# Kernel optimization log

Hardware: AMD Instinct MI355X
Metric: run time of the kernel (lower is better)

Reference implementation:

```python
import jax, jax.numpy as jnp
import numpy as np

B, T, D, H = 2, 2048, 2048, 16
HS = D // H  # head size 128


def setup_inputs() -> dict:
    key = jax.random.key(0)
    ks = jax.random.split(key, 5)
    s = 0.02
    return {
        "x": jax.random.normal(ks[0], (B, T, D), dtype=jnp.float32),
        "wq": jax.random.normal(ks[1], (D, D), dtype=jnp.float32) * s,
        "wk": jax.random.normal(ks[2], (D, D), dtype=jnp.float32) * s,
        "wv": jax.random.normal(ks[3], (D, D), dtype=jnp.float32) * s,
        "wo": jax.random.normal(ks[4], (D, D), dtype=jnp.float32) * s,
    }


def reference(x, wq, wk, wv, wo):
    b, t, d = x.shape
    # projections: nn.Linear(x) = x @ W.T ; here W stored as (out,in)
    q = (x @ wq.T).reshape(b, t, H, HS).transpose(0, 2, 1, 3)  # (B,H,T,HS)
    k = (x @ wk.T).reshape(b, t, H, HS).transpose(0, 2, 1, 3)
    v = (x @ wv.T).reshape(b, t, H, HS).transpose(0, 2, 1, 3)
    scale = 1.0 / np.sqrt(HS).astype(np.float32)
    e = jnp.einsum("bhqd,bhkd->bhqk", q, k) * scale  # (B,H,T,T)
    causal = jnp.tril(jnp.ones((t, t), dtype=bool))
    e = jnp.where(causal[None, None], e, jnp.float32(-jnp.inf))
    alpha = jax.nn.softmax(e, axis=-1)  # dropout=0.0 -> identity
    attn = jnp.einsum("bhqk,bhkd->bhqd", alpha, v)
    attn = attn.transpose(0, 2, 1, 3).reshape(b, t, d)
    return attn @ wo.T
```

## Files before the change

### kernel.cpp

```cpp
#include <hip/hip_runtime.h>
#include <hip/hip_bf16.h>

typedef __bf16 bf16x8 __attribute__((ext_vector_type(8)));
typedef float f32x4 __attribute__((ext_vector_type(4)));
typedef unsigned short u16x8 __attribute__((ext_vector_type(8)));

#define GLDS16(g, s)                                                         \
  __builtin_amdgcn_global_load_lds(                                          \
      (const __attribute__((address_space(1))) void*)(g),                    \
      (__attribute__((address_space(3))) void*)(s), 16, 0, 0)

__device__ __forceinline__ void store1(__hip_bfloat16* p, float v) { *p = __float2bfloat16(v); }
__device__ __forceinline__ void store1(float* p, float v) { *p = v; }

__global__ __launch_bounds__(256) void cast_f32_to_bf16(const float4* __restrict__ in,
                                                        ushort4* __restrict__ out, int n4) {
  int i = blockIdx.x * 256 + threadIdx.x;
  if (i >= n4) return;
  float4 v = in[i];
  union { ushort4 u; __hip_bfloat16 h[4]; } o;
  o.h[0] = __float2bfloat16(v.x);
  o.h[1] = __float2bfloat16(v.y);
  o.h[2] = __float2bfloat16(v.z);
  o.h[3] = __float2bfloat16(v.w);
  out[i] = o.u;
}

__global__ __launch_bounds__(256) void cast4_f32_to_bf16(const float4* __restrict__ w0,
                                                         const float4* __restrict__ w1,
                                                         const float4* __restrict__ w2,
                                                         const float4* __restrict__ w3,
                                                         ushort4* __restrict__ o0,
                                                         ushort4* __restrict__ o1,
                                                         ushort4* __restrict__ o2,
                                                         ushort4* __restrict__ o3, int n4) {
  int i = blockIdx.x * 256 + threadIdx.x;
  if (i >= n4) return;
  int s = blockIdx.y;
  const float4* in = (s == 0) ? w0 : (s == 1) ? w1 : (s == 2) ? w2 : w3;
  ushort4* out = (s == 0) ? o0 : (s == 1) ? o1 : (s == 2) ? o2 : o3;
  float4 v = in[i];
  union { ushort4 u; __hip_bfloat16 h[4]; } o;
  o.h[0] = __float2bfloat16(v.x);
  o.h[1] = __float2bfloat16(v.y);
  o.h[2] = __float2bfloat16(v.z);
  o.h[3] = __float2bfloat16(v.w);
  out[i] = o.u;
}

template <typename OutT>
__global__ __launch_bounds__(512, 2) void gemm256(const __hip_bfloat16* __restrict__ A,
                                                  const __hip_bfloat16* __restrict__ B0,
                                                  const __hip_bfloat16* __restrict__ B1,
                                                  const __hip_bfloat16* __restrict__ B2,
                                                  OutT* __restrict__ C0,
                                                  OutT* __restrict__ C1,
                                                  OutT* __restrict__ C2,
                                                  int nBx, int nBy, int ntPerMat,
                                                  int N, int K) {
  __shared__ __hip_bfloat16 As[3][128 * 64];
  __shared__ __hip_bfloat16 Bs[3][256 * 64];

  const int t = threadIdx.x;
  const int w = t >> 6, l = t & 63;
  const int lr = l & 15, hi = l >> 4;

  const int nwg = nBx * nBy;
  int id = (int)blockIdx.x;
  id = (id & 7) * (nwg >> 3) + (id >> 3);
  const int bx = id / nBy;
  const int by = id % nBy;

  const int sel = bx / ntPerMat;
  const __hip_bfloat16* Bm = (sel == 0) ? B0 : ((sel == 1) ? B1 : B2);
  OutT* Cm = (sel == 0) ? C0 : ((sel == 1) ? C1 : C2);
  const int n0 = (bx - sel * ntPerMat) * 256;
  const int m0 = by * 128;

  const int c0r = t >> 3, cs = t & 7;
  const int c1r = 64 + c0r;
  const __hip_bfloat16* aP0 = A + (size_t)(m0 + c0r) * K + (cs ^ (c0r & 7)) * 8;
  const __hip_bfloat16* aP1 = A + (size_t)(m0 + c1r) * K + (cs ^ (c1r & 7)) * 8;
  const __hip_bfloat16* bP0 = Bm + (size_t)(n0 + c0r) * K + (cs ^ (c0r & 7)) * 8;
  const __hip_bfloat16* bP1 = Bm + (size_t)(n0 + c1r) * K + (cs ^ (c1r & 7)) * 8;
  const size_t HK = (size_t)128 * K;

#define STAGE_T(bb, koff)                                                    \
  do {                                                                       \
    GLDS16(aP0 + (koff), (char*)As[bb] + t * 16);                            \
    GLDS16(aP1 + (koff), (char*)As[bb] + 8192 + t * 16);                     \
    GLDS16(bP0 + (koff), (char*)Bs[bb] + t * 16);                            \
    GLDS16(bP1 + (koff), (char*)Bs[bb] + 8192 + t * 16);                     \
    GLDS16(bP0 + HK + (koff), (char*)Bs[bb] + 16384 + t * 16);               \
    GLDS16(bP1 + HK + (koff), (char*)Bs[bb] + 24576 + t * 16);               \
  } while (0)

  f32x4 acc[2][4][2] = {};
  bf16x8 afA[4][2];
  bf16x8 bqA[2][2], bqB[2][2];
  const int NT = K / 64;
  const int sw = lr & 7;
  const int arow = (w >> 2) * 64;
  const int brow = (w & 3) * 32;

#define RD_A(dst)                                                            \
  _Pragma("unroll") for (int mi = 0; mi < 4; ++mi)                           \
    _Pragma("unroll") for (int kk = 0; kk < 2; ++kk)                         \
      dst[mi][kk] = *(const bf16x8*)((const char*)As[buf] +                  \
          (arow + mi * 16 + lr) * 128 + (((kk * 4 + hi) ^ sw) << 4));
#define RD_B(dst, nh)                                                        \
  _Pragma("unroll") for (int ni = 0; ni < 2; ++ni)                           \
    _Pragma("unroll") for (int kk = 0; kk < 2; ++kk)                         \
      dst[ni][kk] = *(const bf16x8*)((const char*)Bs[buf] +                  \
          ((nh) * 128 + brow + ni * 16 + lr) * 128 + (((kk * 4 + hi) ^ sw) << 4));
#define MFMA_Q(nh, afv, bq)                                                  \
  do {                                                                       \
    __builtin_amdgcn_s_setprio(1);                                           \
    _Pragma("unroll") for (int mi = 0; mi < 4; ++mi)                         \
      _Pragma("unroll") for (int ni = 0; ni < 2; ++ni) {                     \
        acc[nh][mi][ni] = __builtin_amdgcn_mfma_f32_16x16x32_bf16(           \
            afv[mi][0], bq[ni][0], acc[nh][mi][ni], 0, 0, 0);                \
        acc[nh][mi][ni] = __builtin_amdgcn_mfma_f32_16x16x32_bf16(           \
            afv[mi][1], bq[ni][1], acc[nh][mi][ni], 0, 0, 0);                \
      }                                                                      \
    __builtin_amdgcn_s_setprio(0);                                           \
  } while (0)
#define WAITV(n)  asm volatile("s_waitcnt vmcnt(" #n ")" ::: "memory")

  STAGE_T(0, 0);
  STAGE_T(1, 64);

  for (int tt = 0; tt < NT; ++tt) {
    const int buf = tt % 3;

    if (tt + 1 < NT) WAITV(6); else WAITV(0);
    __builtin_amdgcn_s_barrier();

    RD_A(afA);
    RD_B(bqA, 0);
    RD_B(bqB, 1);
    if (tt + 2 < NT) STAGE_T((tt + 2) % 3, (size_t)(tt + 2) * 64);

    MFMA_Q(0, afA, bqA);
    MFMA_Q(1, afA, bqB);
  }
#undef WAITV
#undef MFMA_Q
#undef RD_B
#undef RD_A
#undef STAGE_T

#pragma unroll
  for (int nh = 0; nh < 2; ++nh)
#pragma unroll
    for (int mi = 0; mi < 4; ++mi)
#pragma unroll
      for (int ni = 0; ni < 2; ++ni)
#pragma unroll
        for (int i = 0; i < 4; ++i) {
          size_t idx = (size_t)(m0 + arow + mi * 16 + hi * 4 + i) * N +
                       (n0 + nh * 128 + brow + ni * 16 + lr);
          store1(&Cm[idx], acc[nh][mi][ni][i]);
        }
}

__global__ __launch_bounds__(256, 2) void flash_attn(const __hip_bfloat16* __restrict__ Qg,
                                                     const __hip_bfloat16* __restrict__ Kg,
                                                     const __hip_bfloat16* __restrict__ Vg,
                                                     __hip_bfloat16* __restrict__ Og) {
  __shared__ __hip_bfloat16 Ks[2][64 * 128];
  __shared__ __hip_bfloat16 Vt[128 * 64];

  const int mblk = blockIdx.x;
  const int bh = mblk & 31;
  const int jj = mblk >> 5;
  const int qt = (jj < 8) ? (15 - jj) : (jj - 8);
  const int b = bh >> 4, h = bh & 15;
  const int q0 = qt * 128;
  const int t = threadIdx.x, w = t >> 6, l = t & 63;
  const int lr = l & 15, hi = l >> 4;
  const size_t base = ((size_t)b * 2048) * 2048 + (size_t)h * 128;
  const int nt = 2 * qt + 2;
  const float scale = 0.08838834764831843f;

  const int hi2 = (hi & 1) * 2;
  const int addrA = (((hi2) << 4) | lr) << 2;
  const int addrB = (((hi2 + 1) << 4) | lr) << 2;
  int addr_o[4];
#pragma unroll
  for (int i = 0; i < 4; ++i) addr_o[i] = ((l & 48) | (hi * 4 + i)) << 2;
  const bool hiHigh = (hi >> 1) != 0;

  bf16x8 qf[2][4];
#pragma unroll
  for (int g = 0; g < 2; ++g) {
    const __hip_bfloat16* qrow = Qg + base + (size_t)(q0 + w * 32 + g * 16 + lr) * 2048;
#pragma unroll
    for (int kk = 0; kk < 4; ++kk)
      qf[g][kk] = *(const bf16x8*)(qrow + kk * 32 + hi * 8);
  }

  f32x4 o_acc[2][8] = {};
  float m_run[2] = {-1e30f, -1e30f};
  float l_run[2] = {0.f, 0.f};

  const __hip_bfloat16* kptr[4];
#pragma unroll
  for (int i = 0; i < 4; ++i) {
    int c = i * 256 + t;
    int kr = c >> 4;
    int ke = ((c & 15) ^ (kr & 7)) * 8;
    kptr[i] = Kg + base + (size_t)kr * 2048 + ke;
  }
  const __hip_bfloat16* vptr[2];
#pragma unroll
  for (int it = 0; it < 2; ++it) {
    int kp = it * 16 + w * 4 + hi;
    vptr[it] = Vg + base + (size_t)(kp * 2) * 2048 + lr * 8;
  }

  u16x8 va[2], vb[2];
#pragma unroll
  for (int i = 0; i < 4; ++i)
    GLDS16(kptr[i], (char*)Ks[0] + (i * 256 + t) * 16);
#pragma unroll
  for (int it = 0; it < 2; ++it) {
    va[it] = *(const u16x8*)vptr[it];
    vb[it] = *(const u16x8*)(vptr[it] + 2048);
  }

  for (int kt = 0; kt < nt; ++kt) {
    const int cur = kt & 1;
    const int kb = kt * 64;
    __syncthreads();

#pragma unroll
    for (int it = 0; it < 2; ++it)
#pragma unroll
      for (int j2 = 0; j2 < 8; ++j2) {
        int d = lr * 8 + j2;
        int sw = (lr ^ j2) & 7;
        int off = d * 128 + (((it * 4 + w) ^ sw) << 4) + hi * 4;
        *(unsigned int*)((char*)Vt + off) =
            (unsigned int)va[it][j2] | ((unsigned int)vb[it][j2] << 16);
      }
    if (kt + 1 < nt) {
      const size_t adv = (size_t)(kb + 64) * 2048;
#pragma unroll
      for (int i = 0; i < 4; ++i)
        GLDS16(kptr[i] + adv, (char*)Ks[cur ^ 1] + (i * 256 + t) * 16);
#pragma unroll
      for (int it = 0; it < 2; ++it) {
        va[it] = *(const u16x8*)(vptr[it] + adv);
        vb[it] = *(const u16x8*)(vptr[it] + adv + 2048);
      }
    }
    asm volatile("s_waitcnt lgkmcnt(0)" ::: "memory");
    __builtin_amdgcn_s_barrier();

    if (!(kt == nt - 1 && w < 2)) {
      const char* ks = (const char*)Ks[cur];

      f32x4 st[2][4];
#pragma unroll
      for (int g = 0; g < 2; ++g)
#pragma unroll
        for (int nk = 0; nk < 4; ++nk) { f32x4 z = {}; st[g][nk] = z; }
#pragma unroll
      for (int nk = 0; nk < 4; ++nk)
#pragma unroll
        for (int kk = 0; kk < 4; ++kk) {
          bf16x8 kf = *(const bf16x8*)(ks + (nk * 16 + lr) * 256 +
                                       (((kk * 4 + hi) ^ (lr & 7)) << 4));
#pragma unroll
          for (int g = 0; g < 2; ++g)
            st[g][nk] = __builtin_amdgcn_mfma_f32_16x16x32_bf16(kf, qf[g][kk], st[g][nk], 0, 0, 0);
        }

      const bool maskt = (kt >= nt - 2);
#pragma unroll
      for (int g = 0; g < 2; ++g)
#pragma unroll
        for (int nk = 0; nk < 4; ++nk)
#pragma unroll
          for (int i = 0; i < 4; ++i) {
            float v = st[g][nk][i] * scale;
            if (maskt) {
              int ki = kb + nk * 16 + hi * 4 + i;
              int qi = q0 + w * 32 + g * 16 + lr;
              if (ki > qi) v = -1e30f;
            }
            st[g][nk][i] = v;
          }

      bf16x8 paf[2][2];
#pragma unroll
      for (int g = 0; g < 2; ++g) {
        float t0 = fmaxf(fmaxf(st[g][0][0], st[g][0][1]), fmaxf(st[g][0][2], st[g][0][3]));
        float t1 = fmaxf(fmaxf(st[g][1][0], st[g][1][1]), fmaxf(st[g][1][2], st[g][1][3]));
        float t2 = fmaxf(fmaxf(st[g][2][0], st[g][2][1]), fmaxf(st[g][2][2], st[g][2][3]));
        float t3 = fmaxf(fmaxf(st[g][3][0], st[g][3][1]), fmaxf(st[g][3][2], st[g][3][3]));
        float mx = fmaxf(fmaxf(t0, t1), fmaxf(t2, t3));
        mx = fmaxf(mx, __shfl_xor(mx, 16));
        mx = fmaxf(mx, __shfl_xor(mx, 32));

        if (!__all(mx - m_run[g] <= 8.0f)) {
          float mnew = fmaxf(m_run[g], mx);
          float rs = __expf(m_run[g] - mnew);
          m_run[g] = mnew;
          l_run[g] *= rs;
          int rsi = __float_as_int(rs);
#pragma unroll
          for (int i = 0; i < 4; ++i) {
            float rso = __int_as_float(__builtin_amdgcn_ds_bpermute(addr_o[i], rsi));
#pragma unroll
            for (int nc = 0; nc < 8; ++nc) o_acc[g][nc][i] *= rso;
          }
        }

#pragma unroll
        for (int nk = 0; nk < 4; ++nk)
#pragma unroll
          for (int i = 0; i < 4; ++i)
            st[g][nk][i] = __expf(st[g][nk][i] - m_run[g]);

        float s0 = (st[g][0][0] + st[g][0][1]) + (st[g][0][2] + st[g][0][3]);
        float s1 = (st[g][1][0] + st[g][1][1]) + (st[g][1][2] + st[g][1][3]);
        float s2 = (st[g][2][0] + st[g][2][1]) + (st[g][2][2] + st[g][2][3]);
        float s3 = (st[g][3][0] + st[g][3][1]) + (st[g][3][2] + st[g][3][3]);
        float sm = (s0 + s1) + (s2 + s3);
        sm += __shfl_xor(sm, 16);
        sm += __shfl_xor(sm, 32);
        l_run[g] += sm;

        unsigned pk[4][2];
#pragma unroll
        for (int nk = 0; nk < 4; ++nk) {
          asm("v_cvt_pk_bf16_f32 %0, %1, %2"
              : "=v"(pk[nk][0]) : "v"(st[g][nk][0]), "v"(st[g][nk][1]));
          asm("v_cvt_pk_bf16_f32 %0, %1, %2"
              : "=v"(pk[nk][1]) : "v"(st[g][nk][2]), "v"(st[g][nk][3]));
        }

#pragma unroll
        for (int kk = 0; kk < 2; ++kk) {
          unsigned au[4];
#pragma unroll
          for (int p = 0; p < 4; ++p) {
            int ad = (p < 2) ? addrA : addrB;
            int v0 = __builtin_amdgcn_ds_bpermute(ad, (int)pk[2 * kk][p & 1]);
            int v1 = __builtin_amdgcn_ds_bpermute(ad, (int)pk[2 * kk + 1][p & 1]);
            au[p] = hiHigh ? (unsigned)v1 : (unsigned)v0;
          }
          union { unsigned u[4]; bf16x8 v; } cv;
          cv.u[0] = au[0]; cv.u[1] = au[1]; cv.u[2] = au[2]; cv.u[3] = au[3];
          paf[g][kk] = cv.v;
        }
      }

#pragma unroll
      for (int kk = 0; kk < 2; ++kk)
#pragma unroll
        for (int nc = 0; nc < 8; ++nc) {
          int d = nc * 16 + lr;
          int sw = ((d >> 3) ^ d) & 7;
          bf16x8 vfr = *(const bf16x8*)((const char*)Vt + d * 128 +
                                        (((kk * 4 + hi) ^ sw) << 4));
#pragma unroll
          for (int g = 0; g < 2; ++g)
            o_acc[g][nc] = __builtin_amdgcn_mfma_f32_16x16x32_bf16(paf[g][kk], vfr, o_acc[g][nc], 0, 0, 0);
        }
    }
  }

#pragma unroll
  for (int g = 0; g < 2; ++g) {
    float lo[4];
#pragma unroll
    for (int i = 0; i < 4; ++i)
      lo[i] = __int_as_float(__builtin_amdgcn_ds_bpermute(addr_o[i], __float_as_int(l_run[g])));
#pragma unroll
    for (int nc = 0; nc < 8; ++nc)
#pragma unroll
      for (int i = 0; i < 4; ++i) {
        float val = o_acc[g][nc][i] / lo[i];
        Og[base + (size_t)(q0 + w * 32 + g * 16 + hi * 4 + i) * 2048 + nc * 16 + lr] =
            __float2bfloat16(val);
      }
  }
}

extern "C" void kernel_launch(void* const* d_in, const int* in_sizes, int n_in,
                              void* d_out, int out_size, void* d_ws, size_t ws_size,
                              hipStream_t stream) {
  const float* x  = (const float*)d_in[0];
  const float* wq = (const float*)d_in[1];
  const float* wk = (const float*)d_in[2];
  const float* wv = (const float*)d_in[3];
  const float* wo = (const float*)d_in[4];
  float* out = (float*)d_out;

  const int BT = 4096, D = 2048;
  const size_t ND = (size_t)D * D;
  const size_t NX = (size_t)BT * D;

  __hip_bfloat16* xb  = (__hip_bfloat16*)d_ws;
  __hip_bfloat16* wqb = xb + NX;
  __hip_bfloat16* wkb = wqb + ND;
  __hip_bfloat16* wvb = wkb + ND;
  __hip_bfloat16* wob = wvb + ND;
  __hip_bfloat16* Qb  = wob + ND;
  __hip_bfloat16* Kb  = Qb + NX;
  __hip_bfloat16* Vb  = Kb + NX;
  __hip_bfloat16* Ab  = Vb + NX;

  cast_f32_to_bf16<<<(int)(NX / 4 / 256), 256, 0, stream>>>((const float4*)x, (ushort4*)xb, (int)(NX / 4));
  cast4_f32_to_bf16<<<dim3((int)(ND / 4 / 256), 4), 256, 0, stream>>>(
      (const float4*)wq, (const float4*)wk, (const float4*)wv, (const float4*)wo,
      (ushort4*)wqb, (ushort4*)wkb, (ushort4*)wvb, (ushort4*)wob, (int)(ND / 4));

  gemm256<__hip_bfloat16><<<768, 512, 0, stream>>>(
      xb, wqb, wkb, wvb, Qb, Kb, Vb, 24, 32, 8, D, D);

  flash_attn<<<512, 256, 0, stream>>>(Qb, Kb, Vb, Ab);

  gemm256<float><<<256, 512, 0, stream>>>(
      Ab, wob, wob, wob, out, out, out, 8, 32, 8, D, D);
}
```

Measured before the change: 277.6 us.

## Software-pipeline QK^T in flash attention, simplify GEMM to double buffering, split QKV launches

The flash attention loop now computes the next tile's QK^T scores ahead of the softmax/PV work on the current tile. It double-buffers the V transpose in shared memory so the next V tile can be written while the current one is consumed. The GEMM drops from a 3-stage to a 2-stage LDS pipeline with a full vmcnt(0) wait each iteration, and the fused QKV launch is split into three separate launches. This trades more registers and LDS in attention, plus less load/compute overlap and extra launches in the GEMMs, for more overlap inside attention.

```diff
diff --git a/kernel.cpp b/kernel.cpp
--- a/kernel.cpp
+++ b/kernel.cpp
@@ -51,15 +51,10 @@
 template <typename OutT>
 __global__ __launch_bounds__(512, 2) void gemm256(const __hip_bfloat16* __restrict__ A,
                                                   const __hip_bfloat16* __restrict__ B0,
-                                                  const __hip_bfloat16* __restrict__ B1,
-                                                  const __hip_bfloat16* __restrict__ B2,
                                                   OutT* __restrict__ C0,
-                                                  OutT* __restrict__ C1,
-                                                  OutT* __restrict__ C2,
-                                                  int nBx, int nBy, int ntPerMat,
-                                                  int N, int K) {
-  __shared__ __hip_bfloat16 As[3][128 * 64];
-  __shared__ __hip_bfloat16 Bs[3][256 * 64];
+                                                  int nBx, int nBy, int N, int K) {
+  __shared__ __hip_bfloat16 As[2][128 * 64];
+  __shared__ __hip_bfloat16 Bs[2][256 * 64];
 
   const int t = threadIdx.x;
   const int w = t >> 6, l = t & 63;
@@ -71,18 +66,15 @@
   const int bx = id / nBy;
   const int by = id % nBy;
 
-  const int sel = bx / ntPerMat;
-  const __hip_bfloat16* Bm = (sel == 0) ? B0 : ((sel == 1) ? B1 : B2);
-  OutT* Cm = (sel == 0) ? C0 : ((sel == 1) ? C1 : C2);
-  const int n0 = (bx - sel * ntPerMat) * 256;
+  const int n0 = bx * 256;
   const int m0 = by * 128;
 
   const int c0r = t >> 3, cs = t & 7;
   const int c1r = 64 + c0r;
   const __hip_bfloat16* aP0 = A + (size_t)(m0 + c0r) * K + (cs ^ (c0r & 7)) * 8;
   const __hip_bfloat16* aP1 = A + (size_t)(m0 + c1r) * K + (cs ^ (c1r & 7)) * 8;
-  const __hip_bfloat16* bP0 = Bm + (size_t)(n0 + c0r) * K + (cs ^ (c0r & 7)) * 8;
-  const __hip_bfloat16* bP1 = Bm + (size_t)(n0 + c1r) * K + (cs ^ (c1r & 7)) * 8;
+  const __hip_bfloat16* bP0 = B0 + (size_t)(n0 + c0r) * K + (cs ^ (c0r & 7)) * 8;
+  const __hip_bfloat16* bP1 = B0 + (size_t)(n0 + c1r) * K + (cs ^ (c1r & 7)) * 8;
   const size_t HK = (size_t)128 * K;
 
 #define STAGE_T(bb, koff)                                                    \
@@ -128,19 +120,18 @@
 #define WAITV(n)  asm volatile("s_waitcnt vmcnt(" #n ")" ::: "memory")
 
   STAGE_T(0, 0);
-  STAGE_T(1, 64);
 
   for (int tt = 0; tt < NT; ++tt) {
-    const int buf = tt % 3;
-
-    if (tt + 1 < NT) WAITV(6); else WAITV(0);
+    const int buf = tt & 1, nb = buf ^ 1;
+    const bool stg = (tt + 1 < NT);
+    const size_t ko = (size_t)(tt + 1) * 64;
+
+    WAITV(0);
     __builtin_amdgcn_s_barrier();
-
     RD_A(afA);
     RD_B(bqA, 0);
     RD_B(bqB, 1);
-    if (tt + 2 < NT) STAGE_T((tt + 2) % 3, (size_t)(tt + 2) * 64);
-
+    if (stg) STAGE_T(nb, ko);
     MFMA_Q(0, afA, bqA);
     MFMA_Q(1, afA, bqB);
   }
@@ -160,7 +151,7 @@
         for (int i = 0; i < 4; ++i) {
           size_t idx = (size_t)(m0 + arow + mi * 16 + hi * 4 + i) * N +
                        (n0 + nh * 128 + brow + ni * 16 + lr);
-          store1(&Cm[idx], acc[nh][mi][ni][i]);
+          store1(&C0[idx], acc[nh][mi][ni][i]);
         }
 }
 
@@ -169,7 +160,7 @@
                                                      const __hip_bfloat16* __restrict__ Vg,
                                                      __hip_bfloat16* __restrict__ Og) {
   __shared__ __hip_bfloat16 Ks[2][64 * 128];
-  __shared__ __hip_bfloat16 Vt[128 * 64];
+  __shared__ __hip_bfloat16 Vt[2][128 * 64];
 
   const int mblk = blockIdx.x;
   const int bh = mblk & 31;
@@ -219,7 +210,32 @@
     vptr[it] = Vg + base + (size_t)(kp * 2) * 2048 + lr * 8;
   }
 
+#define WRITE_VT(vbuf, a, bmat)                                              \
+  _Pragma("unroll") for (int it = 0; it < 2; ++it)                           \
+    _Pragma("unroll") for (int j2 = 0; j2 < 8; ++j2) {                       \
+      int d = lr * 8 + j2;                                                   \
+      int swz = (lr ^ j2) & 7;                                               \
+      int off = d * 128 + (((it * 4 + w) ^ swz) << 4) + hi * 4;              \
+      *(unsigned int*)((char*)Vt[vbuf] + off) =                              \
+          (unsigned)a[it][j2] | ((unsigned)bmat[it][j2] << 16);              \
+    }
+#define QK_MFMA(dst, ksbuf)                                                  \
+  do {                                                                       \
+    const char* ks_ = (const char*)Ks[ksbuf];                                \
+    _Pragma("unroll") for (int g = 0; g < 2; ++g)                            \
+      _Pragma("unroll") for (int nk = 0; nk < 4; ++nk) { f32x4 z = {}; dst[g][nk] = z; } \
+    _Pragma("unroll") for (int nk = 0; nk < 4; ++nk)                         \
+      _Pragma("unroll") for (int kk = 0; kk < 4; ++kk) {                     \
+        bf16x8 kf = *(const bf16x8*)(ks_ + (nk * 16 + lr) * 256 +            \
+                                     (((kk * 4 + hi) ^ (lr & 7)) << 4));     \
+        _Pragma("unroll") for (int g = 0; g < 2; ++g)                        \
+          dst[g][nk] = __builtin_amdgcn_mfma_f32_16x16x32_bf16(kf, qf[g][kk], dst[g][nk], 0, 0, 0); \
+      }                                                                      \
+  } while (0)
+
   u16x8 va[2], vb[2];
+  f32x4 st[2][4];
+
 #pragma unroll
   for (int i = 0; i < 4; ++i)
     GLDS16(kptr[i], (char*)Ks[0] + (i * 256 + t) * 16);
@@ -228,55 +244,47 @@
     va[it] = *(const u16x8*)vptr[it];
     vb[it] = *(const u16x8*)(vptr[it] + 2048);
   }
+  asm volatile("s_waitcnt vmcnt(0)" ::: "memory");
+  __builtin_amdgcn_s_barrier();
+  WRITE_VT(0, va, vb);
+  if (nt > 1) {
+    const size_t adv = (size_t)64 * 2048;
+#pragma unroll
+    for (int i = 0; i < 4; ++i)
+      GLDS16(kptr[i] + adv, (char*)Ks[1] + (i * 256 + t) * 16);
+#pragma unroll
+    for (int it = 0; it < 2; ++it) {
+      va[it] = *(const u16x8*)(vptr[it] + adv);
+      vb[it] = *(const u16x8*)(vptr[it] + adv + 2048);
+    }
+  }
+  QK_MFMA(st, 0);
+  asm volatile("s_waitcnt lgkmcnt(0)" ::: "memory");
 
   for (int kt = 0; kt < nt; ++kt) {
-    const int cur = kt & 1;
     const int kb = kt * 64;
-    __syncthreads();
-
-#pragma unroll
-    for (int it = 0; it < 2; ++it)
-#pragma unroll
-      for (int j2 = 0; j2 < 8; ++j2) {
-        int d = lr * 8 + j2;
-        int sw = (lr ^ j2) & 7;
-        int off = d * 128 + (((it * 4 + w) ^ sw) << 4) + hi * 4;
-        *(unsigned int*)((char*)Vt + off) =
-            (unsigned int)va[it][j2] | ((unsigned int)vb[it][j2] << 16);
-      }
-    if (kt + 1 < nt) {
-      const size_t adv = (size_t)(kb + 64) * 2048;
+
+    asm volatile("s_waitcnt vmcnt(4)" ::: "memory");
+    __builtin_amdgcn_s_barrier();
+
+    if (kt + 1 < nt) { WRITE_VT((kt + 1) & 1, va, vb); }
+    if (kt + 2 < nt) {
+      const size_t adv = (size_t)(kb + 128) * 2048;
 #pragma unroll
       for (int i = 0; i < 4; ++i)
-        GLDS16(kptr[i] + adv, (char*)Ks[cur ^ 1] + (i * 256 + t) * 16);
+        GLDS16(kptr[i] + adv, (char*)Ks[kt & 1] + (i * 256 + t) * 16);
 #pragma unroll
       for (int it = 0; it < 2; ++it) {
         va[it] = *(const u16x8*)(vptr[it] + adv);
         vb[it] = *(const u16x8*)(vptr[it] + adv + 2048);
       }
     }
-    asm volatile("s_waitcnt lgkmcnt(0)" ::: "memory");
-    __builtin_amdgcn_s_barrier();
-
-    if (!(kt == nt - 1 && w < 2)) {
-      const char* ks = (const char*)Ks[cur];
-
-      f32x4 st[2][4];
-#pragma unroll
-      for (int g = 0; g < 2; ++g)
-#pragma unroll
-        for (int nk = 0; nk < 4; ++nk) { f32x4 z = {}; st[g][nk] = z; }
-#pragma unroll
-      for (int nk = 0; nk < 4; ++nk)
-#pragma unroll
-        for (int kk = 0; kk < 4; ++kk) {
-          bf16x8 kf = *(const bf16x8*)(ks + (nk * 16 + lr) * 256 +
-                                       (((kk * 4 + hi) ^ (lr & 7)) << 4));
-#pragma unroll
-          for (int g = 0; g < 2; ++g)
-            st[g][nk] = __builtin_amdgcn_mfma_f32_16x16x32_bf16(kf, qf[g][kk], st[g][nk], 0, 0, 0);
-        }
-
+
+    f32x4 stn[2][4];
+    if (kt + 1 < nt) { QK_MFMA(stn, (kt + 1) & 1); }
+
+    const bool active = !(kt == nt - 1 && w < 2);
+    if (active) {
       const bool maskt = (kt >= nt - 2);
 #pragma unroll
       for (int g = 0; g < 2; ++g)
@@ -363,13 +371,21 @@
 #pragma unroll
         for (int nc = 0; nc < 8; ++nc) {
           int d = nc * 16 + lr;
-          int sw = ((d >> 3) ^ d) & 7;
-          bf16x8 vfr = *(const bf16x8*)((const char*)Vt + d * 128 +
-                                        (((kk * 4 + hi) ^ sw) << 4));
+          int swz = ((d >> 3) ^ d) & 7;
+          bf16x8 vfr = *(const bf16x8*)((const char*)Vt[kt & 1] + d * 128 +
+                                        (((kk * 4 + hi) ^ swz) << 4));
 #pragma unroll
           for (int g = 0; g < 2; ++g)
             o_acc[g][nc] = __builtin_amdgcn_mfma_f32_16x16x32_bf16(paf[g][kk], vfr, o_acc[g][nc], 0, 0, 0);
         }
+    }
+
+    asm volatile("s_waitcnt lgkmcnt(0)" ::: "memory");
+    if (kt + 1 < nt) {
+#pragma unroll
+      for (int g = 0; g < 2; ++g)
+#pragma unroll
+        for (int nk = 0; nk < 4; ++nk) st[g][nk] = stn[g][nk];
     }
   }
 
@@ -388,6 +404,8 @@
             __float2bfloat16(val);
       }
   }
+#undef QK_MFMA
+#undef WRITE_VT
 }
 
 extern "C" void kernel_launch(void* const* d_in, const int* in_sizes, int n_in,
@@ -419,11 +437,11 @@
       (const float4*)wq, (const float4*)wk, (const float4*)wv, (const float4*)wo,
       (ushort4*)wqb, (ushort4*)wkb, (ushort4*)wvb, (ushort4*)wob, (int)(ND / 4));
 
-  gemm256<__hip_bfloat16><<<768, 512, 0, stream>>>(
-      xb, wqb, wkb, wvb, Qb, Kb, Vb, 24, 32, 8, D, D);
+  gemm256<__hip_bfloat16><<<256, 512, 0, stream>>>(xb, wqb, Qb, 8, 32, D, D);
+  gemm256<__hip_bfloat16><<<256, 512, 0, stream>>>(xb, wkb, Kb, 8, 32, D, D);
+  gemm256<__hip_bfloat16><<<256, 512, 0, stream>>>(xb, wvb, Vb, 8, 32, D, D);
 
   flash_attn<<<512, 256, 0, stream>>>(Qb, Kb, Vb, Ab);
 
-  gemm256<float><<<256, 512, 0, stream>>>(
-      Ab, wob, wob, wob, out, out, out, 8, 32, 8, D, D);
+  gemm256<float><<<256, 512, 0, stream>>>(Ab, wob, out, 8, 32, D, D);
 }
```

Result: slower. 329.1 us (+18.5%).
